# Kernel optimization log

Hardware: AMD Instinct MI355X
Metric: run time of the kernel (lower is better)

The kernel has to match this reference:

```python
import jax, jax.numpy as jnp
import numpy as np

WS = (7, 7)   # window size
SS = (3, 3)   # shift size
NH = 8        # num heads
DIM = 256
B_, H_, W_ = 16, 112, 112


def _rel_index(wh, ww):
    ch, cw = np.meshgrid(np.arange(wh), np.arange(ww), indexing='ij')
    cf = np.stack([ch, cw]).reshape(2, -1)
    rc = (cf[:, :, None] - cf[:, None, :]).transpose(1, 2, 0)
    rc[:, :, 0] += wh - 1
    rc[:, :, 1] += ww - 1
    rc[:, :, 0] *= 2 * ww - 1
    return rc.sum(-1).reshape(-1)


def _shift_mask(pH, pW, wh, ww, sh, sw):
    m = np.zeros((pH, pW))
    cnt = 0
    for h0, h1 in ((0, pH - wh), (pH - wh, pH - sh), (pH - sh, pH)):
        for w0, w1 in ((0, pW - ww), (pW - ww, pW - sw), (pW - sw, pW)):
            m[h0:h1, w0:w1] = cnt
            cnt += 1
    m = m.reshape(pH // wh, wh, pW // ww, ww).transpose(0, 2, 1, 3).reshape(-1, wh * ww)
    d = m[:, None, :] - m[:, :, None]  # (nW, N, N), [w,i,j] = m[w,j]-m[w,i]
    return np.where(d != 0, -100.0, 0.0).astype(np.float32)


def _partition(x, wh, ww):
    B, H, W, C = x.shape
    x = x.reshape(B, H // wh, wh, W // ww, ww, C).transpose(0, 1, 3, 2, 4, 5)
    return x.reshape(B * (H // wh) * (W // ww), wh * ww, C)


def _unpartition(x, B, H, W, wh, ww):
    C = x.shape[-1]
    x = x.reshape(B, H // wh, W // ww, wh, ww, C).transpose(0, 1, 3, 2, 4, 5)
    return x.reshape(B, H, W, C)


def setup_inputs() -> dict:
    key = jax.random.key(0)
    ks = jax.random.split(key, 12)
    D = DIM
    inp = {
        'Q': jax.random.normal(ks[0], (B_, H_, W_, D), jnp.float32),
        'K': jax.random.normal(ks[1], (B_, H_, W_, D), jnp.float32),
        'V': jax.random.normal(ks[2], (B_, H_, W_, D), jnp.float32),
        'Qw': jax.random.normal(ks[3], (D, D), jnp.float32) * 0.02,
        'Qb': jax.random.normal(ks[4], (D,), jnp.float32) * 0.02,
        'Kw': jax.random.normal(ks[5], (D, D), jnp.float32) * 0.02,
        'Kb': jax.random.normal(ks[6], (D,), jnp.float32) * 0.02,
        'Vw': jax.random.normal(ks[7], (D, D), jnp.float32) * 0.02,
        'Vb': jax.random.normal(ks[8], (D,), jnp.float32) * 0.02,
        'Pw': jax.random.normal(ks[9], (D, D), jnp.float32) * 0.02,
        'Pb': jax.random.normal(ks[10], (D,), jnp.float32) * 0.02,
        'rpb_table': jax.random.normal(ks[11], ((2 * WS[0] - 1) * (2 * WS[1] - 1), NH), jnp.float32) * 0.02,
        'rp_index': jnp.asarray(_rel_index(WS[0], WS[1]), jnp.int32),
    }
    return inp


def reference(Q, K, V, Qw, Qb, Kw, Kb, Vw, Vb, Pw, Pb, rpb_table, rp_index):
    wh, ww = WS
    nh = NH
    B, H, W, C = Q.shape
    N = wh * ww
    hd = C // nh
    pad_b = (wh - H % wh) % wh
    pad_r = (ww - W % ww) % ww
    if pad_b or pad_r:
        pad = ((0, 0), (0, pad_b), (0, pad_r), (0, 0))
        Q, K, V = jnp.pad(Q, pad), jnp.pad(K, pad), jnp.pad(V, pad)
    pH, pW = H + pad_b, W + pad_r
    sh = 0 if wh >= pH else SS[0]
    sw = 0 if ww >= pW else SS[1]
    shifted = (sh + sw) > 0
    if shifted:
        Q = jnp.roll(Q, (-sh, -sw), (1, 2))
        K = jnp.roll(K, (-sh, -sw), (1, 2))
        V = jnp.roll(V, (-sh, -sw), (1, 2))
    xq = _partition(Q, wh, ww)  # (B*nW, N, C)
    xk = _partition(K, wh, ww)
    xv = _partition(V, wh, ww)
    q = (xq @ Qw.T + Qb).reshape(-1, N, nh, hd).transpose(0, 2, 1, 3) * (hd ** -0.5)
    k = (xk @ Kw.T + Kb).reshape(-1, N, nh, hd).transpose(0, 2, 1, 3)
    v = (xv @ Vw.T + Vb).reshape(-1, N, nh, hd).transpose(0, 2, 1, 3)
    bias = rpb_table[rp_index].reshape(N, N, nh).transpose(2, 0, 1)  # (nh, N, N)
    attn = jnp.einsum('bhnd,bhmd->bhnm', q, k) + bias[None]
    if shifted:
        mask = jnp.asarray(_shift_mask(pH, pW, wh, ww, sh, sw))  # (nW, N, N)
        nW = (pH // wh) * (pW // ww)
        attn = attn.reshape(B, nW, nh, N, N) + mask[None, :, None]
        attn = attn.reshape(-1, nh, N, N)
    attn = jax.nn.softmax(attn, axis=-1)
    x = jnp.einsum('bhnm,bhmd->bhnd', attn, v).transpose(0, 2, 1, 3).reshape(-1, N, C)
    x = x @ Pw.T + Pb
    x = _unpartition(x, B, pH, pW, wh, ww)
    if shifted:
        x = jnp.roll(x, (sh, sw), (1, 2))
    return x[:, :H, :W, :]
```

## Files before the change

### kernel.cpp

```cpp
#include <hip/hip_runtime.h>


typedef short  bf16x4_t __attribute__((ext_vector_type(4)));
typedef short  bf16x8_t __attribute__((ext_vector_type(8)));
typedef float  f32x4_t  __attribute__((ext_vector_type(4)));
typedef int    i32x4_t  __attribute__((ext_vector_type(4)));

#define HH    112
#define WWDIM 112
#define NTOK  49
#define NWIN  4096
#define SHIFT 3

__device__ __forceinline__ unsigned short f2bf(float f) {
  unsigned u = __builtin_bit_cast(unsigned, f);
  u += 0x7FFFu + ((u >> 16) & 1u);
  return (unsigned short)(u >> 16);
}

__device__ __forceinline__ bf16x8_t ld8(const unsigned short* p) {
  return __builtin_bit_cast(bf16x8_t, *reinterpret_cast<const i32x4_t*>(p));
}

__device__ __forceinline__ bf16x4_t pack4(float a, float b, float c, float d) {
  union { unsigned short u[4]; bf16x4_t v; } t;
  t.u[0] = f2bf(a); t.u[1] = f2bf(b); t.u[2] = f2bf(c); t.u[3] = f2bf(d);
  return t.v;
}

__device__ __forceinline__ int swzi(int row, int col, int rowElems) {
  int by = col << 1;
  int sb = (((by >> 4) ^ (row & 7)) << 4) | (by & 15);
  return row * rowElems + (sb >> 1);
}

__global__ void prep_kernel(const float* __restrict__ Qw, const float* __restrict__ Kw,
                            const float* __restrict__ Vw, const float* __restrict__ Pw,
                            const float* __restrict__ rpb, const int* __restrict__ rpi,
                            unsigned short* __restrict__ wbf, float* __restrict__ biasT) {
  int idx = blockIdx.x * 256 + threadIdx.x;
  if (idx < 4 * 65536) {
    int which = idx >> 16, e = idx & 65535;
    const float* s = (which == 0) ? Qw : (which == 1) ? Kw : (which == 2) ? Vw : Pw;
    wbf[idx] = f2bf(s[e]);
  }
  if (idx < 8 * NTOK * NTOK) {
    int h = idx / (NTOK * NTOK), ij = idx % (NTOK * NTOK);
    int i = ij / NTOK, j = ij - (ij / NTOK) * NTOK;
    biasT[h * (NTOK * NTOK) + j * NTOK + i] = rpb[rpi[ij] * 8 + h];
  }
}

#define GLOAD(SRC)                                                            \
  do {                                                                        \
    _Pragma("unroll") for (int it = 0; it < 8; ++it) {                        \
      g[it] = ((wid + (it << 3)) < NTOK)                                      \
                  ? *reinterpret_cast<const float4*>((SRC) + goff[it])        \
                  : make_float4(0.f, 0.f, 0.f, 0.f);                          \
    }                                                                         \
  } while (0)

#define XWRITE()                                                              \
  do {                                                                        \
    _Pragma("unroll") for (int it = 0; it < 8; ++it) {                        \
      unsigned v0 = (unsigned)f2bf(g[it].x) | ((unsigned)f2bf(g[it].y) << 16);\
      unsigned v1 = (unsigned)f2bf(g[it].z) | ((unsigned)f2bf(g[it].w) << 16);\
      *reinterpret_cast<uint2*>(                                              \
          &Xs[swzi(wid + (it << 3), lane << 2, 256)]) = make_uint2(v0, v1);   \
    }                                                                         \
  } while (0)

#define WHOIST(PH)                                                            \
  do {                                                                        \
    const unsigned short* W_ = wbf + ((PH) << 16);                            \
    _Pragma("unroll") for (int ks = 0; ks < 8; ++ks)                          \
        _Pragma("unroll") for (int t = 0; t < 2; ++t)                         \
            bw[ks][t] =                                                       \
        ld8(&W_[(((wid << 5) + (t << 4) + lo) << 8) + (ks << 5) + kof]);      \
  } while (0)

__global__ __launch_bounds__(512, 2) void fused_kernel(
    const float* __restrict__ Qin, const float* __restrict__ Kin, const float* __restrict__ Vin,
    const float* __restrict__ Qbv, const float* __restrict__ Kbv, const float* __restrict__ Vbv,
    const float* __restrict__ Pbv,
    const unsigned short* __restrict__ wbf, const float* __restrict__ biasT,
    float* __restrict__ out) {
  __shared__ unsigned short Xs[64 * 256];

  const int blk = blockIdx.x, tid = threadIdx.x;
  const int lane = tid & 63, wid = tid >> 6;
  const int b = blk >> 8, wi = (blk >> 4) & 15, wj = blk & 15;
  const int lo = lane & 15, hi = lane >> 4;
  const int g4 = hi << 2, kof = hi << 3;

  unsigned goff[8];
#pragma unroll
  for (int it = 0; it < 8; ++it) {
    int row = wid + (it << 3);
    unsigned off = 0;
    if (row < NTOK) {
      int i = row / 7, j = row - i * 7;
      int h_ = wi * 7 + i + SHIFT; if (h_ >= HH) h_ -= HH;
      int w_ = wj * 7 + j + SHIFT; if (w_ >= WWDIM) w_ -= WWDIM;
      off = ((unsigned)((b * HH + h_) * WWDIM + w_) << 8) + (lane << 2);
    }
    goff[it] = off;
  }

  float4 g[8];
  bf16x8_t bw[8][2];
  bf16x4_t qf[2][4], kf[2][4], vf[4][2];

  GLOAD(Qin);
  WHOIST(0);
  XWRITE();
  __syncthreads();

#pragma unroll
  for (int ph = 0; ph < 2; ++ph) {
    GLOAD(ph == 0 ? Kin : Vin);
    f32x4_t acc[2][4];
#pragma unroll
    for (int a = 0; a < 2; ++a)
#pragma unroll
      for (int c = 0; c < 4; ++c) acc[a][c] = (f32x4_t){0.f, 0.f, 0.f, 0.f};
#pragma unroll
    for (int ks = 0; ks < 8; ++ks) {
      const int kk = (ks << 5) + kof;
      bf16x8_t xb[4];
#pragma unroll
      for (int nj = 0; nj < 4; ++nj) xb[nj] = ld8(&Xs[swzi((nj << 4) + lo, kk, 256)]);
#pragma unroll
      for (int mi = 0; mi < 2; ++mi)
#pragma unroll
        for (int nj = 0; nj < 4; ++nj)
          acc[mi][nj] = __builtin_amdgcn_mfma_f32_16x16x32_bf16(bw[ks][mi], xb[nj], acc[mi][nj], 0, 0, 0);
    }
    const float* bias = (ph == 0) ? Qbv : Kbv;
    const float scale = (ph == 0) ? 0.17677669529663687f : 1.0f;
    bf16x4_t (*dst)[4] = (ph == 0) ? qf : kf;
#pragma unroll
    for (int mi = 0; mi < 2; ++mi) {
      const float4 bb = *reinterpret_cast<const float4*>(bias + (wid << 5) + (mi << 4) + g4);
#pragma unroll
      for (int nj = 0; nj < 4; ++nj)
        dst[mi][nj] = pack4((acc[mi][nj][0] + bb.x) * scale, (acc[mi][nj][1] + bb.y) * scale,
                            (acc[mi][nj][2] + bb.z) * scale, (acc[mi][nj][3] + bb.w) * scale);
    }
    __syncthreads();
    WHOIST(ph + 1);
    XWRITE();
    __syncthreads();
  }

  {
    f32x4_t acc[4][2];
#pragma unroll
    for (int a = 0; a < 4; ++a)
#pragma unroll
      for (int c = 0; c < 2; ++c) acc[a][c] = (f32x4_t){0.f, 0.f, 0.f, 0.f};
#pragma unroll
    for (int ks = 0; ks < 8; ++ks) {
      const int kk = (ks << 5) + kof;
      bf16x8_t xa[4];
#pragma unroll
      for (int mi = 0; mi < 4; ++mi) xa[mi] = ld8(&Xs[swzi((mi << 4) + lo, kk, 256)]);
#pragma unroll
      for (int mi = 0; mi < 4; ++mi)
#pragma unroll
        for (int t = 0; t < 2; ++t)
          acc[mi][t] = __builtin_amdgcn_mfma_f32_16x16x32_bf16(xa[mi], bw[ks][t], acc[mi][t], 0, 0, 0);
    }
    float bbv[2];
#pragma unroll
    for (int t = 0; t < 2; ++t) bbv[t] = Vbv[(wid << 5) + (t << 4) + lo];
#pragma unroll
    for (int mi = 0; mi < 4; ++mi)
#pragma unroll
      for (int t = 0; t < 2; ++t)
        vf[mi][t] = pack4(acc[mi][t][0] + bbv[t], acc[mi][t][1] + bbv[t],
                          acc[mi][t][2] + bbv[t], acc[mi][t][3] + bbv[t]);
  }
  WHOIST(3);

  const bool wi15 = (wi == 15), wj15 = (wj == 15);
  unsigned kbi = 0, kbj = 0, kval = 0;
#pragma unroll
  for (int njk = 0; njk < 4; ++njk)
#pragma unroll
    for (int rg = 0; rg < 4; ++rg) {
      int kt = (njk << 4) + g4 + rg;
      if (kt < NTOK) {
        int ti = kt / 7, tj = kt - (kt / 7) * 7;
        unsigned bit = 1u << (njk * 4 + rg);
        kval |= bit;
        if (ti >= 4) kbi |= bit;
        if (tj >= 4) kbj |= bit;
      }
    }

  f32x4_t st[4][4];
  __builtin_amdgcn_s_setprio(1);
#pragma unroll
  for (int njk = 0; njk < 4; ++njk)
#pragma unroll
    for (int njq = 0; njq < 4; ++njq) {
      st[njk][njq] = __builtin_amdgcn_mfma_f32_16x16x16bf16_1k(
          kf[0][njk], qf[0][njq], (f32x4_t){0.f, 0.f, 0.f, 0.f}, 0, 0, 0);
      st[njk][njq] = __builtin_amdgcn_mfma_f32_16x16x16bf16_1k(
          kf[1][njk], qf[1][njq], st[njk][njq], 0, 0, 0);
    }
  __builtin_amdgcn_s_setprio(0);

  const float* bh = biasT + wid * (NTOK * NTOK);
  bf16x4_t pf[4][4];
#pragma unroll
  for (int njq = 0; njq < 4; ++njq) {
    const int qt = (njq << 4) + lo;
    const bool qv = qt < NTOK;
    const int sqt = qv ? qt : 0;
    const int qti = sqt / 7, qtj = sqt - (sqt / 7) * 7;
    const bool qbi = qti >= 4, qbj = qtj >= 4;
    float vals[4][4];
    float m = -3e38f;
#pragma unroll
    for (int njk = 0; njk < 4; ++njk)
#pragma unroll
      for (int rg = 0; rg < 4; ++rg) {
        const int bit = njk * 4 + rg;
        const int kt = (njk << 4) + g4 + rg;
        const bool valid = qv && ((kval >> bit) & 1u);
        float v = st[njk][njq][rg] + bh[(valid ? kt : 0) * NTOK + sqt];
        if (wi15 && (qbi != (bool)((kbi >> bit) & 1u))) v -= 100.f;
        if (wj15 && (qbj != (bool)((kbj >> bit) & 1u))) v -= 100.f;
        v = valid ? v : -1e30f;
        vals[njk][rg] = v;
        m = fmaxf(m, v);
      }
    m = fmaxf(m, __shfl_xor(m, 16));
    m = fmaxf(m, __shfl_xor(m, 32));
    float sum = 0.f;
#pragma unroll
    for (int njk = 0; njk < 4; ++njk)
#pragma unroll
      for (int rg = 0; rg < 4; ++rg) {
        const float e = __expf(vals[njk][rg] - m);
        vals[njk][rg] = e;
        sum += e;
      }
    sum += __shfl_xor(sum, 16);
    sum += __shfl_xor(sum, 32);
    const float inv = 1.f / sum;
#pragma unroll
    for (int njk = 0; njk < 4; ++njk)
      pf[njk][njq] = pack4(vals[njk][0] * inv, vals[njk][1] * inv,
                           vals[njk][2] * inv, vals[njk][3] * inv);
  }

  f32x4_t o[2][4];
#pragma unroll
  for (int a = 0; a < 2; ++a)
#pragma unroll
    for (int c = 0; c < 4; ++c) o[a][c] = (f32x4_t){0.f, 0.f, 0.f, 0.f};
  __builtin_amdgcn_s_setprio(1);
#pragma unroll
  for (int mi = 0; mi < 4; ++mi)
#pragma unroll
    for (int t = 0; t < 2; ++t)
#pragma unroll
      for (int njq = 0; njq < 4; ++njq)
        o[t][njq] = __builtin_amdgcn_mfma_f32_16x16x16bf16_1k(vf[mi][t], pf[mi][njq], o[t][njq], 0, 0, 0);
  __builtin_amdgcn_s_setprio(0);

  __syncthreads();
#pragma unroll
  for (int t = 0; t < 2; ++t)
#pragma unroll
    for (int njq = 0; njq < 4; ++njq) {
      const int qt = (njq << 4) + lo;
      const int ch0 = (wid << 5) + (t << 4) + g4;
      unsigned u0 = (unsigned)f2bf(o[t][njq][0]) | ((unsigned)f2bf(o[t][njq][1]) << 16);
      unsigned u1 = (unsigned)f2bf(o[t][njq][2]) | ((unsigned)f2bf(o[t][njq][3]) << 16);
      *reinterpret_cast<uint2*>(&Xs[swzi(qt, ch0, 256)]) = make_uint2(u0, u1);
    }
  __syncthreads();

  f32x4_t y[2][4];
#pragma unroll
  for (int a = 0; a < 2; ++a)
#pragma unroll
    for (int c = 0; c < 4; ++c) y[a][c] = (f32x4_t){0.f, 0.f, 0.f, 0.f};
#pragma unroll
  for (int ks = 0; ks < 8; ++ks) {
    const int kk = (ks << 5) + kof;
    bf16x8_t xb[4];
#pragma unroll
    for (int nj = 0; nj < 4; ++nj) xb[nj] = ld8(&Xs[swzi((nj << 4) + lo, kk, 256)]);
#pragma unroll
    for (int mi = 0; mi < 2; ++mi)
#pragma unroll
      for (int nj = 0; nj < 4; ++nj)
        y[mi][nj] = __builtin_amdgcn_mfma_f32_16x16x32_bf16(bw[ks][mi], xb[nj], y[mi][nj], 0, 0, 0);
  }
  float4 pb[2];
#pragma unroll
  for (int mi = 0; mi < 2; ++mi)
    pb[mi] = *reinterpret_cast<const float4*>(Pbv + (wid << 5) + (mi << 4) + g4);
#pragma unroll
  for (int nj = 0; nj < 4; ++nj) {
    const int tok = (nj << 4) + lo;
    if (tok < NTOK) {
      const int i = tok / 7, j = tok - (tok / 7) * 7;
      int h_ = wi * 7 + i + SHIFT; if (h_ >= HH) h_ -= HH;
      int w_ = wj * 7 + j + SHIFT; if (w_ >= WWDIM) w_ -= WWDIM;
      float* ob = out + ((size_t)((b * HH + h_) * WWDIM + w_) << 8);
#pragma unroll
      for (int mi = 0; mi < 2; ++mi) {
        const int ch0 = (wid << 5) + (mi << 4) + g4;
        *reinterpret_cast<float4*>(ob + ch0) =
            make_float4(y[mi][nj][0] + pb[mi].x, y[mi][nj][1] + pb[mi].y,
                        y[mi][nj][2] + pb[mi].z, y[mi][nj][3] + pb[mi].w);
      }
    }
  }
}

extern "C" void kernel_launch(void* const* d_in, const int* in_sizes, int n_in,
                              void* d_out, int out_size, void* d_ws, size_t ws_size,
                              hipStream_t stream) {
  const float* Q   = (const float*)d_in[0];
  const float* K   = (const float*)d_in[1];
  const float* V   = (const float*)d_in[2];
  const float* Qw  = (const float*)d_in[3];
  const float* Qb  = (const float*)d_in[4];
  const float* Kw  = (const float*)d_in[5];
  const float* Kb  = (const float*)d_in[6];
  const float* Vw  = (const float*)d_in[7];
  const float* Vb  = (const float*)d_in[8];
  const float* Pw  = (const float*)d_in[9];
  const float* Pb  = (const float*)d_in[10];
  const float* rpb = (const float*)d_in[11];
  const int*   rpi = (const int*)d_in[12];

  unsigned short* wbf = (unsigned short*)d_ws;
  float* biasT = (float*)(wbf + 4 * 65536);

  const size_t need = (size_t)4 * 65536 * 2 + (size_t)8 * NTOK * NTOK * 4;
  if (ws_size < need) return;

  prep_kernel<<<1024, 256, 0, stream>>>(Qw, Kw, Vw, Pw, rpb, rpi, wbf, biasT);
  fused_kernel<<<NWIN, 512, 0, stream>>>(Q, K, V, Qb, Kb, Vb, Pb, wbf, biasT,
                                         (float*)d_out);
}
```

Baseline: 459.6 us.

## Stream weights double-buffered per k-step and compute scores per query tile to cut VGPRs

```diff
diff --git a/kernel.cpp b/kernel.cpp
--- a/kernel.cpp
+++ b/kernel.cpp
@@ -70,16 +70,14 @@
     }                                                                         \
   } while (0)
 
-#define WHOIST(PH)                                                            \
+#define WLOAD(WP, KS, S)                                                      \
   do {                                                                        \
-    const unsigned short* W_ = wbf + ((PH) << 16);                            \
-    _Pragma("unroll") for (int ks = 0; ks < 8; ++ks)                          \
-        _Pragma("unroll") for (int t = 0; t < 2; ++t)                         \
-            bw[ks][t] =                                                       \
-        ld8(&W_[(((wid << 5) + (t << 4) + lo) << 8) + (ks << 5) + kof]);      \
+    _Pragma("unroll") for (int t = 0; t < 2; ++t)                             \
+      bwr[S][t] = ld8(&(WP)[(((wid << 5) + (t << 4) + lo) << 8) +             \
+                            ((KS) << 5) + kof]);                              \
   } while (0)
 
-__global__ __launch_bounds__(512, 2) void fused_kernel(
+__global__ __launch_bounds__(512, 4) void fused_kernel(
     const float* __restrict__ Qin, const float* __restrict__ Kin, const float* __restrict__ Vin,
     const float* __restrict__ Qbv, const float* __restrict__ Kbv, const float* __restrict__ Vbv,
     const float* __restrict__ Pbv,
@@ -108,24 +106,26 @@
   }
 
   float4 g[8];
-  bf16x8_t bw[8][2];
+  bf16x8_t bwr[2][2];
   bf16x4_t qf[2][4], kf[2][4], vf[4][2];
 
   GLOAD(Qin);
-  WHOIST(0);
   XWRITE();
   __syncthreads();
 
 #pragma unroll
   for (int ph = 0; ph < 2; ++ph) {
     GLOAD(ph == 0 ? Kin : Vin);
+    const unsigned short* W_ = wbf + (ph << 16);
     f32x4_t acc[2][4];
 #pragma unroll
     for (int a = 0; a < 2; ++a)
 #pragma unroll
       for (int c = 0; c < 4; ++c) acc[a][c] = (f32x4_t){0.f, 0.f, 0.f, 0.f};
+    WLOAD(W_, 0, 0);
 #pragma unroll
     for (int ks = 0; ks < 8; ++ks) {
+      if (ks < 7) WLOAD(W_, ks + 1, (ks + 1) & 1);
       const int kk = (ks << 5) + kof;
       bf16x8_t xb[4];
 #pragma unroll
@@ -134,7 +134,7 @@
       for (int mi = 0; mi < 2; ++mi)
 #pragma unroll
         for (int nj = 0; nj < 4; ++nj)
-          acc[mi][nj] = __builtin_amdgcn_mfma_f32_16x16x32_bf16(bw[ks][mi], xb[nj], acc[mi][nj], 0, 0, 0);
+          acc[mi][nj] = __builtin_amdgcn_mfma_f32_16x16x32_bf16(bwr[ks & 1][mi], xb[nj], acc[mi][nj], 0, 0, 0);
     }
     const float* bias = (ph == 0) ? Qbv : Kbv;
     const float scale = (ph == 0) ? 0.17677669529663687f : 1.0f;
@@ -148,19 +148,21 @@
                             (acc[mi][nj][2] + bb.z) * scale, (acc[mi][nj][3] + bb.w) * scale);
     }
     __syncthreads();
-    WHOIST(ph + 1);
     XWRITE();
     __syncthreads();
   }
 
   {
+    const unsigned short* W_ = wbf + (2 << 16);
     f32x4_t acc[4][2];
 #pragma unroll
     for (int a = 0; a < 4; ++a)
 #pragma unroll
       for (int c = 0; c < 2; ++c) acc[a][c] = (f32x4_t){0.f, 0.f, 0.f, 0.f};
+    WLOAD(W_, 0, 0);
 #pragma unroll
     for (int ks = 0; ks < 8; ++ks) {
+      if (ks < 7) WLOAD(W_, ks + 1, (ks + 1) & 1);
       const int kk = (ks << 5) + kof;
       bf16x8_t xa[4];
 #pragma unroll
@@ -169,7 +171,7 @@
       for (int mi = 0; mi < 4; ++mi)
 #pragma unroll
         for (int t = 0; t < 2; ++t)
-          acc[mi][t] = __builtin_amdgcn_mfma_f32_16x16x32_bf16(xa[mi], bw[ks][t], acc[mi][t], 0, 0, 0);
+          acc[mi][t] = __builtin_amdgcn_mfma_f32_16x16x32_bf16(xa[mi], bwr[ks & 1][t], acc[mi][t], 0, 0, 0);
     }
     float bbv[2];
 #pragma unroll
@@ -181,7 +183,6 @@
         vf[mi][t] = pack4(acc[mi][t][0] + bbv[t], acc[mi][t][1] + bbv[t],
                           acc[mi][t][2] + bbv[t], acc[mi][t][3] + bbv[t]);
   }
-  WHOIST(3);
 
   const bool wi15 = (wi == 15), wj15 = (wj == 15);
   unsigned kbi = 0, kbj = 0, kval = 0;
@@ -199,23 +200,21 @@
       }
     }
 
-  f32x4_t st[4][4];
-  __builtin_amdgcn_s_setprio(1);
-#pragma unroll
-  for (int njk = 0; njk < 4; ++njk)
-#pragma unroll
-    for (int njq = 0; njq < 4; ++njq) {
-      st[njk][njq] = __builtin_amdgcn_mfma_f32_16x16x16bf16_1k(
-          kf[0][njk], qf[0][njq], (f32x4_t){0.f, 0.f, 0.f, 0.f}, 0, 0, 0);
-      st[njk][njq] = __builtin_amdgcn_mfma_f32_16x16x16bf16_1k(
-          kf[1][njk], qf[1][njq], st[njk][njq], 0, 0, 0);
-    }
-  __builtin_amdgcn_s_setprio(0);
-
   const float* bh = biasT + wid * (NTOK * NTOK);
   bf16x4_t pf[4][4];
 #pragma unroll
   for (int njq = 0; njq < 4; ++njq) {
+    f32x4_t stc[4];
+    __builtin_amdgcn_s_setprio(1);
+#pragma unroll
+    for (int njk = 0; njk < 4; ++njk) {
+      stc[njk] = __builtin_amdgcn_mfma_f32_16x16x16bf16_1k(
+          kf[0][njk], qf[0][njq], (f32x4_t){0.f, 0.f, 0.f, 0.f}, 0, 0, 0);
+      stc[njk] = __builtin_amdgcn_mfma_f32_16x16x16bf16_1k(
+          kf[1][njk], qf[1][njq], stc[njk], 0, 0, 0);
+    }
+    __builtin_amdgcn_s_setprio(0);
+
     const int qt = (njq << 4) + lo;
     const bool qv = qt < NTOK;
     const int sqt = qv ? qt : 0;
@@ -230,7 +229,7 @@
         const int bit = njk * 4 + rg;
         const int kt = (njk << 4) + g4 + rg;
         const bool valid = qv && ((kval >> bit) & 1u);
-        float v = st[njk][njq][rg] + bh[(valid ? kt : 0) * NTOK + sqt];
+        float v = stc[njk][rg] + bh[(valid ? kt : 0) * NTOK + sqt];
         if (wi15 && (qbi != (bool)((kbi >> bit) & 1u))) v -= 100.f;
         if (wj15 && (qbj != (bool)((kbj >> bit) & 1u))) v -= 100.f;
         v = valid ? v : -1e30f;
@@ -285,41 +284,46 @@
     }
   __syncthreads();
 
-  f32x4_t y[2][4];
-#pragma unroll
-  for (int a = 0; a < 2; ++a)
-#pragma unroll
-    for (int c = 0; c < 4; ++c) y[a][c] = (f32x4_t){0.f, 0.f, 0.f, 0.f};
-#pragma unroll
-  for (int ks = 0; ks < 8; ++ks) {
-    const int kk = (ks << 5) + kof;
-    bf16x8_t xb[4];
-#pragma unroll
-    for (int nj = 0; nj < 4; ++nj) xb[nj] = ld8(&Xs[swzi((nj << 4) + lo, kk, 256)]);
+  {
+    const unsigned short* W_ = wbf + (3 << 16);
+    f32x4_t y[2][4];
+#pragma unroll
+    for (int a = 0; a < 2; ++a)
+#pragma unroll
+      for (int c = 0; c < 4; ++c) y[a][c] = (f32x4_t){0.f, 0.f, 0.f, 0.f};
+    WLOAD(W_, 0, 0);
+#pragma unroll
+    for (int ks = 0; ks < 8; ++ks) {
+      if (ks < 7) WLOAD(W_, ks + 1, (ks + 1) & 1);
+      const int kk = (ks << 5) + kof;
+      bf16x8_t xb[4];
+#pragma unroll
+      for (int nj = 0; nj < 4; ++nj) xb[nj] = ld8(&Xs[swzi((nj << 4) + lo, kk, 256)]);
+#pragma unroll
+      for (int mi = 0; mi < 2; ++mi)
+#pragma unroll
+        for (int nj = 0; nj < 4; ++nj)
+          y[mi][nj] = __builtin_amdgcn_mfma_f32_16x16x32_bf16(bwr[ks & 1][mi], xb[nj], y[mi][nj], 0, 0, 0);
+    }
+    float4 pb[2];
 #pragma unroll
     for (int mi = 0; mi < 2; ++mi)
-#pragma unroll
-      for (int nj = 0; nj < 4; ++nj)
-        y[mi][nj] = __builtin_amdgcn_mfma_f32_16x16x32_bf16(bw[ks][mi], xb[nj], y[mi][nj], 0, 0, 0);
-  }
-  float4 pb[2];
-#pragma unroll
-  for (int mi = 0; mi < 2; ++mi)
-    pb[mi] = *reinterpret_cast<const float4*>(Pbv + (wid << 5) + (mi << 4) + g4);
-#pragma unroll
-  for (int nj = 0; nj < 4; ++nj) {
-    const int tok = (nj << 4) + lo;
-    if (tok < NTOK) {
-      const int i = tok / 7, j = tok - (tok / 7) * 7;
-      int h_ = wi * 7 + i + SHIFT; if (h_ >= HH) h_ -= HH;
-      int w_ = wj * 7 + j + SHIFT; if (w_ >= WWDIM) w_ -= WWDIM;
-      float* ob = out + ((size_t)((b * HH + h_) * WWDIM + w_) << 8);
-#pragma unroll
-      for (int mi = 0; mi < 2; ++mi) {
-        const int ch0 = (wid << 5) + (mi << 4) + g4;
-        *reinterpret_cast<float4*>(ob + ch0) =
-            make_float4(y[mi][nj][0] + pb[mi].x, y[mi][nj][1] + pb[mi].y,
-                        y[mi][nj][2] + pb[mi].z, y[mi][nj][3] + pb[mi].w);
+      pb[mi] = *reinterpret_cast<const float4*>(Pbv + (wid << 5) + (mi << 4) + g4);
+#pragma unroll
+    for (int nj = 0; nj < 4; ++nj) {
+      const int tok = (nj << 4) + lo;
+      if (tok < NTOK) {
+        const int i = tok / 7, j = tok - (tok / 7) * 7;
+        int h_ = wi * 7 + i + SHIFT; if (h_ >= HH) h_ -= HH;
+        int w_ = wj * 7 + j + SHIFT; if (w_ >= WWDIM) w_ -= WWDIM;
+        float* ob = out + ((size_t)((b * HH + h_) * WWDIM + w_) << 8);
+#pragma unroll
+        for (int mi = 0; mi < 2; ++mi) {
+          const int ch0 = (wid << 5) + (mi << 4) + g4;
+          *reinterpret_cast<float4*>(ob + ch0) =
+              make_float4(y[mi][nj][0] + pb[mi].x, y[mi][nj][1] + pb[mi].y,
+                          y[mi][nj][2] + pb[mi].z, y[mi][nj][3] + pb[mi].w);
+        }
       }
     }
   }
```

Measured after the change: 513.3 us. +11.7%, slower.
